# Optimization experiments

Measured on AMD Instinct MI355X. Metric: run time of the kernel, lower is better.

## Reference

```python
import jax, jax.numpy as jnp
import numpy as np

B, S, E, H, V, OOV = 128, 400, 512, 512, 50257, 50
VEXT = V + OOV


def setup_inputs() -> dict:
    key = jax.random.key(0)
    ks = jax.random.split(key, 20)
    w = lambda k, shp: (0.02 * jax.random.normal(k, shp)).astype(jnp.float32)
    return {
        'input_emb': jax.random.normal(ks[0], (B, 1, E), jnp.float32),
        'input_feed': jax.random.normal(ks[1], (B, 1, H), jnp.float32),
        'hidden': jax.random.normal(ks[2], (1, B, H), jnp.float32),
        'context': jax.random.normal(ks[3], (1, B, H), jnp.float32),
        'states': jax.random.normal(ks[4], (B, S, H), jnp.float32),
        'states_features': jax.random.normal(ks[5], (B, S, H), jnp.float32),
        'source_mask': jnp.ones((B, S), jnp.float32),
        'coverage': jnp.zeros((B, S), jnp.float32),
        'source_ids': jax.random.randint(ks[6], (B, S), 0, VEXT, jnp.int32),
        'W_ic': w(ks[7], (E, H + E)), 'b_ic': jnp.zeros((E,), jnp.float32),
        'W_ih': w(ks[8], (4 * H, E)), 'W_hh': w(ks[9], (4 * H, H)),
        'b_ih': jnp.zeros((4 * H,), jnp.float32), 'b_hh': jnp.zeros((4 * H,), jnp.float32),
        'W_dec': w(ks[10], (H, H)), 'b_att': jnp.zeros((H,), jnp.float32),
        'v_att': w(ks[11], (H,)), 'w_c': w(ks[12], (1,)),
        'W_out': w(ks[13], (H, 2 * H)), 'b_out': jnp.zeros((H,), jnp.float32),
        'W_pg': w(ks[14], (1, H)), 'b_pg': jnp.zeros((1,), jnp.float32),
        'W_v': w(ks[15], (V, H)), 'b_v': jnp.zeros((V,), jnp.float32),
    }


def reference(input_emb, input_feed, hidden, context, states, states_features,
              source_mask, coverage, source_ids,
              W_ic, b_ic, W_ih, W_hh, b_ih, b_hh,
              W_dec, b_att, v_att, w_c, W_out, b_out,
              W_pg, b_pg, W_v, b_v):
    # x = input_context(cat(input_emb, input_feed))  -> [B,1,E]
    x = jnp.concatenate([input_emb, input_feed], axis=2) @ W_ic.T + b_ic
    # single LSTM step (PyTorch gate order i,f,g,o)
    h0, c0 = hidden[0], context[0]                      # [B,H]
    gates = x[:, 0] @ W_ih.T + b_ih + h0 @ W_hh.T + b_hh
    i, f, g, o = jnp.split(gates, 4, axis=-1)
    i, f, o = jax.nn.sigmoid(i), jax.nn.sigmoid(f), jax.nn.sigmoid(o)
    c1 = f * c0 + i * jnp.tanh(g)
    h1 = o * jnp.tanh(c1)                               # rnn_output [B,H]
    # coverage attention
    dec_fea = h1 @ W_dec.T + b_att                      # [B,H]
    e = jnp.tanh(states_features + dec_fea[:, None, :] + w_c * coverage[..., None]) @ v_att  # [B,S]
    e = jnp.where(source_mask > 0, e, jnp.float32(-1e9))
    attn = jax.nn.softmax(e, axis=-1) * source_mask
    attn = attn / (attn.sum(-1, keepdims=True) + 1e-12)  # [B,S]
    ctx = jnp.einsum('bs,bsh->bh', attn, states)
    dec_out = jnp.concatenate([h1, ctx], axis=-1) @ W_out.T + b_out  # decoder_output [B,H]
    coverage_new = coverage + attn
    # pointer-generator mixing
    p_gen = jax.nn.sigmoid(dec_out @ W_pg.T + b_pg)     # [B,1]
    vocab_dist = p_gen * jax.nn.softmax(dec_out @ W_v.T + b_v, axis=-1)  # [B,V]
    ext = jnp.zeros((B, VEXT), vocab_dist.dtype).at[:, :V].set(vocab_dist)
    attn_dist = (1.0 - p_gen) * attn                    # [B,S]
    final = ext.at[jnp.arange(B)[:, None], source_ids].add(attn_dist)  # scatter_add over vocab
    final_dist = final[:, None, :]                      # [B,1,VEXT]
    return (final_dist, p_gen, attn, coverage_new, h1[None], c1[None], dec_out[:, None, :])
```

## Files before the change

### kernel.cpp

```cpp
#include <hip/hip_runtime.h>
#include <hip/hip_bf16.h>

#define B_   128
#define S_   400
#define H_   512
#define V_   50257
#define VX_  50307

#define OFF_FINAL 0
#define OFF_PGEN  6439296
#define OFF_ATTN  6439424
#define OFF_COV   6490624
#define OFF_H1    6541824
#define OFF_C1    6607360
#define OFF_DEC   6672896

typedef __attribute__((ext_vector_type(8))) short bf16x8;
typedef __attribute__((ext_vector_type(4))) float f32x4;

static __device__ __forceinline__ float sigmoid_f(float x) {
    return 1.0f / (1.0f + __expf(-x));
}
static __device__ __forceinline__ float tanh_f(float x) {
    return 1.0f - 2.0f / (__expf(2.0f * x) + 1.0f);
}
static __device__ __forceinline__ unsigned int pk2(float x, float y) {
    union { __hip_bfloat162 h; unsigned int u; } cv;
    cv.h = __float22bfloat162_rn(make_float2(x, y));
    return cv.u;
}

template <int NT>
__global__ __launch_bounds__(256) void gemm_mfma(
    const float* __restrict__ A1, const float* __restrict__ W1, int ldw1, int kwo1,
    const float* __restrict__ A2, const float* __restrict__ W2, int ldw2, int kwo2,
    const float* __restrict__ bias1, const float* __restrict__ bias2,
    float* __restrict__ C, int N)
{
    __shared__ __align__(16) unsigned short As[128 * 40];
    __shared__ __align__(16) unsigned short Ws[NT * 16 * 40];
    const int tid  = threadIdx.x;
    const int bn0  = blockIdx.x * (NT * 16);
    const int lane = tid & 63;
    const int wv   = tid >> 6;
    const int quad = lane >> 4;
    const int col  = lane & 15;

    f32x4 acc[2][NT];
#pragma unroll
    for (int i = 0; i < 2; ++i)
#pragma unroll
        for (int j = 0; j < NT; ++j) acc[i][j] = (f32x4){0.f, 0.f, 0.f, 0.f};

    const int ar = tid >> 1;
    const int ac = (tid & 1) << 4;
    const int wr = (NT == 8) ? (tid >> 1) : (tid >> 2);
    const int wc = (NT == 8) ? ((tid & 1) << 4) : ((tid & 3) << 3);
    const int wrg = (bn0 + wr < N) ? (bn0 + wr) : (N - 1);

    const int nph = (A2 != nullptr) ? 2 : 1;
    const int nsteps = nph << 4;
    const float* ApB[2];
    const float* WpB[2];
    ApB[0] = A1 + (long)ar * 512 + ac;
    WpB[0] = W1 + (long)wrg * ldw1 + kwo1 + wc;
    ApB[1] = A2 ? (A2 + (long)ar * 512 + ac) : ApB[0];
    WpB[1] = W2 ? (W2 + (long)wrg * ldw2 + kwo2 + wc) : WpB[0];

    float4 aC[4], wC[NT / 2], aN[4], wN[NT / 2];

    auto fetch = [&](int s, float4* a, float4* w) {
        const int ph = s >> 4;
        const int k0 = (s & 15) << 5;
        const float* Ap = ApB[ph] + k0;
        const float* Wp = WpB[ph] + k0;
#pragma unroll
        for (int i = 0; i < 4; ++i) a[i] = *(const float4*)(Ap + i * 4);
#pragma unroll
        for (int i = 0; i < NT / 2; ++i) w[i] = *(const float4*)(Wp + i * 4);
    };

    fetch(0, aC, wC);
    for (int s = 0; s < nsteps; ++s) {
        __syncthreads();
        uint4* apd = (uint4*)&As[ar * 40 + ac];
        apd[0] = make_uint4(pk2(aC[0].x, aC[0].y), pk2(aC[0].z, aC[0].w),
                            pk2(aC[1].x, aC[1].y), pk2(aC[1].z, aC[1].w));
        apd[1] = make_uint4(pk2(aC[2].x, aC[2].y), pk2(aC[2].z, aC[2].w),
                            pk2(aC[3].x, aC[3].y), pk2(aC[3].z, aC[3].w));
        uint4* wpd = (uint4*)&Ws[wr * 40 + wc];
        wpd[0] = make_uint4(pk2(wC[0].x, wC[0].y), pk2(wC[0].z, wC[0].w),
                            pk2(wC[1].x, wC[1].y), pk2(wC[1].z, wC[1].w));
        if (NT == 8)
            wpd[1] = make_uint4(pk2(wC[2].x, wC[2].y), pk2(wC[2].z, wC[2].w),
                                pk2(wC[3].x, wC[3].y), pk2(wC[3].z, wC[3].w));
        __syncthreads();

        if (s + 1 < nsteps) fetch(s + 1, aN, wN);

        const bf16x8 aF0 = *(const bf16x8*)&As[(wv * 32 + col) * 40 + quad * 8];
        const bf16x8 aF1 = *(const bf16x8*)&As[(wv * 32 + 16 + col) * 40 + quad * 8];
#pragma unroll
        for (int ni = 0; ni < NT; ++ni) {
            const bf16x8 bF = *(const bf16x8*)&Ws[(ni * 16 + col) * 40 + quad * 8];
            acc[0][ni] = __builtin_amdgcn_mfma_f32_16x16x32_bf16(aF0, bF, acc[0][ni], 0, 0, 0);
            acc[1][ni] = __builtin_amdgcn_mfma_f32_16x16x32_bf16(aF1, bF, acc[1][ni], 0, 0, 0);
        }
#pragma unroll
        for (int i = 0; i < 4; ++i) aC[i] = aN[i];
#pragma unroll
        for (int i = 0; i < NT / 2; ++i) wC[i] = wN[i];
    }

#pragma unroll
    for (int mi = 0; mi < 2; ++mi) {
#pragma unroll
        for (int ni = 0; ni < NT; ++ni) {
            const int n = bn0 + ni * 16 + col;
            if (n < N) {
                float bv = bias1[n];
                if (bias2) bv += bias2[n];
#pragma unroll
                for (int r = 0; r < 4; ++r) {
                    const int m = wv * 32 + mi * 16 + quad * 4 + r;
                    C[(long)m * N + n] = acc[mi][ni][r] + bv;
                }
            }
        }
    }
}

__global__ __launch_bounds__(256) void lstm_cell(
    const float* __restrict__ gates, const float* __restrict__ c0,
    float* __restrict__ h1, float* __restrict__ c1)
{
    const int idx = blockIdx.x * 256 + threadIdx.x;
    const int b = idx >> 9, h = idx & 511;
    const float* g = gates + ((long)b << 11);
    const float gi = sigmoid_f(g[h]);
    const float gf = sigmoid_f(g[h + 512]);
    const float gg = tanh_f(g[h + 1024]);
    const float go = sigmoid_f(g[h + 1536]);
    const float c = gf * c0[idx] + gi * gg;
    c1[idx] = c;
    h1[idx] = go * tanh_f(c);
}

__global__ __launch_bounds__(256) void attn_scores(
    const float* __restrict__ sfeat, const float* __restrict__ decfea,
    const float* __restrict__ cov, const float* __restrict__ wc,
    const float* __restrict__ vatt, float* __restrict__ e)
{
    const int lane = threadIdx.x & 63;
    const int pair = blockIdx.x * 4 + (threadIdx.x >> 6);
    const int b = pair / 400;
    const float cc = wc[0] * cov[pair];
    const float* sp = sfeat + ((long)pair << 9) + (lane << 3);
    const float* dp = decfea + (b << 9) + (lane << 3);
    const float* vp = vatt + (lane << 3);
    const float4 s0 = *(const float4*)sp, s1 = *(const float4*)(sp + 4);
    const float4 d0 = *(const float4*)dp, d1 = *(const float4*)(dp + 4);
    const float4 v0 = *(const float4*)vp, v1 = *(const float4*)(vp + 4);
    float acc = tanh_f(s0.x + d0.x + cc) * v0.x
              + tanh_f(s0.y + d0.y + cc) * v0.y
              + tanh_f(s0.z + d0.z + cc) * v0.z
              + tanh_f(s0.w + d0.w + cc) * v0.w
              + tanh_f(s1.x + d1.x + cc) * v1.x
              + tanh_f(s1.y + d1.y + cc) * v1.y
              + tanh_f(s1.z + d1.z + cc) * v1.z
              + tanh_f(s1.w + d1.w + cc) * v1.w;
#pragma unroll
    for (int off = 32; off > 0; off >>= 1) acc += __shfl_down(acc, off);
    if (lane == 0) e[pair] = acc;
}

__global__ __launch_bounds__(256) void attn_softmax(
    const float* __restrict__ e, const float* __restrict__ mask,
    const float* __restrict__ cov,
    float* __restrict__ attn, float* __restrict__ covnew, float* __restrict__ ctx)
{
    __shared__ float sm[4], sps[4], spms[4];
    const int b = blockIdx.x, tid = threadIdx.x;
    ctx[(b << 9) + tid] = 0.f;
    ctx[(b << 9) + 256 + tid] = 0.f;

    float vals[2], msk[2];
    float m = -3.0e38f;
#pragma unroll
    for (int it = 0; it < 2; ++it) {
        const int s = tid + (it << 8);
        float mk = 0.f, v = -3.0e38f;
        if (s < 400) {
            mk = mask[b * 400 + s];
            v = (mk > 0.f) ? e[b * 400 + s] : -1.0e9f;
        }
        vals[it] = v; msk[it] = mk;
        m = fmaxf(m, v);
    }
#pragma unroll
    for (int off = 32; off > 0; off >>= 1) m = fmaxf(m, __shfl_down(m, off));
    if ((tid & 63) == 0) sm[tid >> 6] = m;
    __syncthreads();
    const float M = fmaxf(fmaxf(sm[0], sm[1]), fmaxf(sm[2], sm[3]));

    float p[2], sp = 0.f, spm = 0.f;
#pragma unroll
    for (int it = 0; it < 2; ++it) {
        const int s = tid + (it << 8);
        float pv = 0.f;
        if (s < 400) pv = __expf(vals[it] - M);
        p[it] = pv; sp += pv; spm += pv * msk[it];
    }
#pragma unroll
    for (int off = 32; off > 0; off >>= 1) {
        sp += __shfl_down(sp, off);
        spm += __shfl_down(spm, off);
    }
    if ((tid & 63) == 0) { sps[tid >> 6] = sp; spms[tid >> 6] = spm; }
    __syncthreads();
    const float SP = sps[0] + sps[1] + sps[2] + sps[3];
    const float SPM = spms[0] + spms[1] + spms[2] + spms[3];
    const float inv = 1.0f / (SPM + 1e-12f * SP);
#pragma unroll
    for (int it = 0; it < 2; ++it) {
        const int s = tid + (it << 8);
        if (s < 400) {
            const float a = p[it] * msk[it] * inv;
            attn[b * 400 + s] = a;
            covnew[b * 400 + s] = cov[b * 400 + s] + a;
        }
    }
}

__global__ __launch_bounds__(256) void ctx_kernel(
    const float* __restrict__ attn, const float* __restrict__ states,
    float* __restrict__ ctx)
{
    const int bx = blockIdx.x;
    const int b = bx >> 2, chunk = bx & 3;
    const int tid = threadIdx.x;
    const int c = tid & 127;
    const int sh = tid >> 7;
    const int s0 = chunk * 100 + sh;
    const float* base = states + (long)b * 400 * 512;
    float4 acc = make_float4(0.f, 0.f, 0.f, 0.f);
    for (int i = 0; i < 50; ++i) {
        const int s = s0 + (i << 1);
        const float a = attn[b * 400 + s];
        const float4 st = *(const float4*)(base + (long)s * 512 + (c << 2));
        acc.x = fmaf(a, st.x, acc.x);
        acc.y = fmaf(a, st.y, acc.y);
        acc.z = fmaf(a, st.z, acc.z);
        acc.w = fmaf(a, st.w, acc.w);
    }
    float* cp = ctx + (b << 9) + (c << 2);
    atomicAdd(cp + 0, acc.x);
    atomicAdd(cp + 1, acc.y);
    atomicAdd(cp + 2, acc.z);
    atomicAdd(cp + 3, acc.w);
}

__global__ __launch_bounds__(64) void pgen_kernel(
    const float* __restrict__ dec_out, const float* __restrict__ wpg,
    const float* __restrict__ bpg, float* __restrict__ pgen)
{
    const int b = blockIdx.x, lane = threadIdx.x;
    const float* dp = dec_out + (b << 9) + (lane << 3);
    const float* wp = wpg + (lane << 3);
    const float4 d0 = *(const float4*)dp, d1 = *(const float4*)(dp + 4);
    const float4 w0 = *(const float4*)wp, w1 = *(const float4*)(wp + 4);
    float acc = d0.x * w0.x + d0.y * w0.y + d0.z * w0.z + d0.w * w0.w
              + d1.x * w1.x + d1.y * w1.y + d1.z * w1.z + d1.w * w1.w;
#pragma unroll
    for (int off = 32; off > 0; off >>= 1) acc += __shfl_down(acc, off);
    if (lane == 0) pgen[b] = sigmoid_f(acc + bpg[0]);
}

__global__ __launch_bounds__(256) void row_stats_part(
    const float* __restrict__ logits, float* __restrict__ pm, float* __restrict__ ps)
{
    __shared__ float sred[4];
    const int b = blockIdx.y, cx = blockIdx.x, tid = threadIdx.x;
    const int v0 = cx * 6283;
    const int v1 = (v0 + 6283 < V_) ? (v0 + 6283) : V_;
    const float* row = logits + (long)b * V_;

    float m = -3.0e38f;
    for (int v = v0 + tid; v < v1; v += 256) m = fmaxf(m, row[v]);
#pragma unroll
    for (int off = 32; off > 0; off >>= 1) m = fmaxf(m, __shfl_down(m, off));
    if ((tid & 63) == 0) sred[tid >> 6] = m;
    __syncthreads();
    const float M = fmaxf(fmaxf(sred[0], sred[1]), fmaxf(sred[2], sred[3]));
    __syncthreads();

    float s = 0.f;
    for (int v = v0 + tid; v < v1; v += 256) s += __expf(row[v] - M);
#pragma unroll
    for (int off = 32; off > 0; off >>= 1) s += __shfl_down(s, off);
    if ((tid & 63) == 0) sred[tid >> 6] = s;
    __syncthreads();
    if (tid == 0) {
        pm[b * 8 + cx] = M;
        ps[b * 8 + cx] = sred[0] + sred[1] + sred[2] + sred[3];
    }
}

__global__ __launch_bounds__(128) void row_stats_fin(
    const float* __restrict__ pm, const float* __restrict__ ps,
    float* __restrict__ rmax, float* __restrict__ rsum)
{
    const int b = threadIdx.x;
    float M = -3.0e38f;
#pragma unroll
    for (int i = 0; i < 8; ++i) M = fmaxf(M, pm[b * 8 + i]);
    float S = 0.f;
#pragma unroll
    for (int i = 0; i < 8; ++i) S += ps[b * 8 + i] * __expf(pm[b * 8 + i] - M);
    rmax[b] = M;
    rsum[b] = S;
}

__global__ __launch_bounds__(256) void final_write(
    const float* __restrict__ logits, const float* __restrict__ rmax,
    const float* __restrict__ rsum, const float* __restrict__ pgen,
    float* __restrict__ final)
{
    const int b = blockIdx.y;
    const int v0 = (blockIdx.x * 256 + threadIdx.x) << 2;
    if (v0 >= VX_) return;
    const float M = rmax[b];
    const float sc = pgen[b] / rsum[b];
    const float* row = logits + (long)b * V_;
    float* out = final + (long)b * VX_ + v0;
#pragma unroll
    for (int j = 0; j < 4; ++j) {
        const int v = v0 + j;
        if (v < VX_) out[j] = (v < V_) ? __expf(row[v] - M) * sc : 0.f;
    }
}

__global__ __launch_bounds__(256) void scatter_kernel(
    const int* __restrict__ ids, const float* __restrict__ attn,
    const float* __restrict__ pgen, float* __restrict__ final)
{
    const int s = blockIdx.x * 256 + threadIdx.x;
    const int b = blockIdx.y;
    if (s < 400) {
        const float v = (1.0f - pgen[b]) * attn[b * 400 + s];
        atomicAdd(final + (long)b * VX_ + ids[b * 400 + s], v);
    }
}

extern "C" void kernel_launch(void* const* d_in, const int* in_sizes, int n_in,
                              void* d_out, int out_size, void* d_ws, size_t ws_size,
                              hipStream_t stream)
{
    const float* input_emb  = (const float*)d_in[0];
    const float* input_feed = (const float*)d_in[1];
    const float* hidden     = (const float*)d_in[2];
    const float* context    = (const float*)d_in[3];
    const float* states     = (const float*)d_in[4];
    const float* sfeat      = (const float*)d_in[5];
    const float* mask       = (const float*)d_in[6];
    const float* cov        = (const float*)d_in[7];
    const int*   src_ids    = (const int*)d_in[8];
    const float* W_ic  = (const float*)d_in[9];
    const float* b_ic  = (const float*)d_in[10];
    const float* W_ih  = (const float*)d_in[11];
    const float* W_hh  = (const float*)d_in[12];
    const float* b_ih  = (const float*)d_in[13];
    const float* b_hh  = (const float*)d_in[14];
    const float* W_dec = (const float*)d_in[15];
    const float* b_att = (const float*)d_in[16];
    const float* v_att = (const float*)d_in[17];
    const float* w_c   = (const float*)d_in[18];
    const float* W_out = (const float*)d_in[19];
    const float* b_out = (const float*)d_in[20];
    const float* W_pg  = (const float*)d_in[21];
    const float* b_pg  = (const float*)d_in[22];
    const float* W_v   = (const float*)d_in[23];
    const float* b_v   = (const float*)d_in[24];

    float* out = (float*)d_out;
    float* o_final = out + OFF_FINAL;
    float* o_pgen  = out + OFF_PGEN;
    float* o_attn  = out + OFF_ATTN;
    float* o_cov   = out + OFF_COV;
    float* o_h1    = out + OFF_H1;
    float* o_c1    = out + OFF_C1;
    float* o_dec   = out + OFF_DEC;

    float* ws = (float*)d_ws;
    float* w_x      = ws;
    float* w_gates  = ws + 65536;
    float* w_decfea = ws + 327680;
    float* w_e      = ws + 393216;
    float* w_ctx    = ws + 444416;
    float* w_logits = ws + 509952;
    float* w_rmax   = ws + 6942848;
    float* w_rsum   = ws + 6942976;
    float* w_pm     = ws + 6943104;
    float* w_ps     = ws + 6944128;

    const dim3 blk(256);
    gemm_mfma<4><<<8, blk, 0, stream>>>(input_emb, W_ic, 1024, 0,
                                        input_feed, W_ic, 1024, 512,
                                        b_ic, nullptr, w_x, 512);
    gemm_mfma<4><<<32, blk, 0, stream>>>(w_x, W_ih, 512, 0,
                                         hidden, W_hh, 512, 0,
                                         b_ih, b_hh, w_gates, 2048);
    lstm_cell<<<256, blk, 0, stream>>>(w_gates, context, o_h1, o_c1);
    gemm_mfma<4><<<8, blk, 0, stream>>>(o_h1, W_dec, 512, 0,
                                        nullptr, nullptr, 0, 0,
                                        b_att, nullptr, w_decfea, 512);
    attn_scores<<<12800, blk, 0, stream>>>(sfeat, w_decfea, cov, w_c, v_att, w_e);
    attn_softmax<<<128, blk, 0, stream>>>(w_e, mask, cov, o_attn, o_cov, w_ctx);
    ctx_kernel<<<512, blk, 0, stream>>>(o_attn, states, w_ctx);
    gemm_mfma<4><<<8, blk, 0, stream>>>(o_h1, W_out, 1024, 0,
                                        w_ctx, W_out, 1024, 512,
                                        b_out, nullptr, o_dec, 512);
    pgen_kernel<<<128, dim3(64), 0, stream>>>(o_dec, W_pg, b_pg, o_pgen);
    gemm_mfma<8><<<393, blk, 0, stream>>>(o_dec, W_v, 512, 0,
                                          nullptr, nullptr, 0, 0,
                                          b_v, nullptr, w_logits, 50257);
    row_stats_part<<<dim3(8, 128), blk, 0, stream>>>(w_logits, w_pm, w_ps);
    row_stats_fin<<<1, dim3(128), 0, stream>>>(w_pm, w_ps, w_rmax, w_rsum);
    final_write<<<dim3(50, 128), blk, 0, stream>>>(w_logits, w_rmax, w_rsum, o_pgen, o_final);
    scatter_kernel<<<dim3(2, 128), blk, 0, stream>>>(src_ids, o_attn, o_pgen, o_final);
}
```

Measured before the change: 521.8 us.

## Split-K small GEMMs, fuse gates with LSTM cell, fold p_gen into decoder GEMM

Adds split-K over gridDim.y for the small 128-row GEMMs (input_context, W_dec, W_out), accumulating with atomics into buffers zeroed by a new kernel. The gates GEMM and LSTM cell are fused so each block computes the i/f/g/o columns for 32 hidden units and applies the cell directly, removing the gates round trip. p_gen's dot product is folded into the W_out GEMM epilogue via atomics, the row_stats_fin kernel is merged into final_write, and the vocab GEMM switches from NT=8 to NT=4 with twice the blocks. The aim is more parallelism for tiny GEMMs and fewer launches, at the cost of float atomics (nondeterministic summation order) and an extra zeroing launch.

Result: faster. 492.1 us (-5.7%).

```diff
diff --git a/kernel.cpp b/kernel.cpp
--- a/kernel.cpp
+++ b/kernel.cpp
@@ -30,12 +30,22 @@
     return cv.u;
 }
 
+__global__ __launch_bounds__(256) void zero_bufs(
+    float* __restrict__ a, float* __restrict__ b, float* __restrict__ c,
+    float* __restrict__ d)
+{
+    const int i = blockIdx.x * 256 + threadIdx.x;
+    a[i] = 0.f; b[i] = 0.f; c[i] = 0.f;
+    if (i < 128) d[i] = 0.f;
+}
+
 template <int NT>
 __global__ __launch_bounds__(256) void gemm_mfma(
     const float* __restrict__ A1, const float* __restrict__ W1, int ldw1, int kwo1,
     const float* __restrict__ A2, const float* __restrict__ W2, int ldw2, int kwo2,
-    const float* __restrict__ bias1, const float* __restrict__ bias2,
-    float* __restrict__ C, int N)
+    const float* __restrict__ bias1,
+    float* __restrict__ C, int N,
+    const float* __restrict__ wpg, float* __restrict__ pgen_acc)
 {
     __shared__ __align__(16) unsigned short As[128 * 40];
     __shared__ __align__(16) unsigned short Ws[NT * 16 * 40];
@@ -58,8 +68,11 @@
     const int wc = (NT == 8) ? ((tid & 1) << 4) : ((tid & 3) << 3);
     const int wrg = (bn0 + wr < N) ? (bn0 + wr) : (N - 1);
 
-    const int nph = (A2 != nullptr) ? 2 : 1;
-    const int nsteps = nph << 4;
+    const int Ktot = (A2 != nullptr) ? 1024 : 512;
+    const int KC   = Ktot / gridDim.y;
+    const int kg0  = blockIdx.y * KC;
+    const int nsteps = KC >> 5;
+
     const float* ApB[2];
     const float* WpB[2];
     ApB[0] = A1 + (long)ar * 512 + ac;
@@ -70,8 +83,9 @@
     float4 aC[4], wC[NT / 2], aN[4], wN[NT / 2];
 
     auto fetch = [&](int s, float4* a, float4* w) {
-        const int ph = s >> 4;
-        const int k0 = (s & 15) << 5;
+        const int kg = kg0 + (s << 5);
+        const int ph = kg >> 9;
+        const int k0 = kg & 511;
         const float* Ap = ApB[ph] + k0;
         const float* Wp = WpB[ph] + k0;
 #pragma unroll
@@ -112,38 +126,143 @@
         for (int i = 0; i < NT / 2; ++i) wC[i] = wN[i];
     }
 
+    const bool split = (gridDim.y > 1);
+    const bool addb  = (!split) || (blockIdx.y == 0);
+    float pgp[2][4];
+#pragma unroll
+    for (int i = 0; i < 2; ++i)
+#pragma unroll
+        for (int r = 0; r < 4; ++r) pgp[i][r] = 0.f;
+
 #pragma unroll
     for (int mi = 0; mi < 2; ++mi) {
 #pragma unroll
         for (int ni = 0; ni < NT; ++ni) {
             const int n = bn0 + ni * 16 + col;
             if (n < N) {
-                float bv = bias1[n];
-                if (bias2) bv += bias2[n];
+                const float bv = addb ? bias1[n] : 0.f;
+                const float wpv = wpg ? wpg[n] : 0.f;
 #pragma unroll
                 for (int r = 0; r < 4; ++r) {
                     const int m = wv * 32 + mi * 16 + quad * 4 + r;
-                    C[(long)m * N + n] = acc[mi][ni][r] + bv;
+                    const float v = acc[mi][ni][r] + bv;
+                    if (split) atomicAdd(&C[(long)m * N + n], v);
+                    else       C[(long)m * N + n] = v;
+                    pgp[mi][r] += v * wpv;
                 }
             }
         }
     }
-}
-
-__global__ __launch_bounds__(256) void lstm_cell(
-    const float* __restrict__ gates, const float* __restrict__ c0,
+    if (wpg) {
+#pragma unroll
+        for (int mi = 0; mi < 2; ++mi)
+#pragma unroll
+            for (int r = 0; r < 4; ++r) {
+                float v = pgp[mi][r];
+                v += __shfl_xor(v, 1); v += __shfl_xor(v, 2);
+                v += __shfl_xor(v, 4); v += __shfl_xor(v, 8);
+                if (col == 0) {
+                    const int m = wv * 32 + mi * 16 + quad * 4 + r;
+                    atomicAdd(&pgen_acc[m], v);
+                }
+            }
+    }
+}
+
+__global__ __launch_bounds__(256) void gates_lstm(
+    const float* __restrict__ x, const float* __restrict__ h0,
+    const float* __restrict__ Wih, const float* __restrict__ Whh,
+    const float* __restrict__ bih, const float* __restrict__ bhh,
+    const float* __restrict__ c0,
     float* __restrict__ h1, float* __restrict__ c1)
 {
-    const int idx = blockIdx.x * 256 + threadIdx.x;
-    const int b = idx >> 9, h = idx & 511;
-    const float* g = gates + ((long)b << 11);
-    const float gi = sigmoid_f(g[h]);
-    const float gf = sigmoid_f(g[h + 512]);
-    const float gg = tanh_f(g[h + 1024]);
-    const float go = sigmoid_f(g[h + 1536]);
-    const float c = gf * c0[idx] + gi * gg;
-    c1[idx] = c;
-    h1[idx] = go * tanh_f(c);
+    __shared__ __align__(16) unsigned short As[128 * 40];
+    __shared__ __align__(16) unsigned short Ws[128 * 40];
+    const int tid  = threadIdx.x;
+    const int bh0  = blockIdx.x * 32;
+    const int lane = tid & 63;
+    const int wv   = tid >> 6;
+    const int quad = lane >> 4;
+    const int col  = lane & 15;
+
+    f32x4 acc[2][8];
+#pragma unroll
+    for (int i = 0; i < 2; ++i)
+#pragma unroll
+        for (int j = 0; j < 8; ++j) acc[i][j] = (f32x4){0.f, 0.f, 0.f, 0.f};
+
+    const int ar = tid >> 1;
+    const int ac = (tid & 1) << 4;
+    const int wr = tid >> 1;
+    const int wc = (tid & 1) << 4;
+    const int wrow = ((wr >> 5) << 9) + bh0 + (wr & 31);
+
+    const float* ApB[2] = { x + (long)ar * 512 + ac, h0 + (long)ar * 512 + ac };
+    const float* WpB[2] = { Wih + (long)wrow * 512 + wc, Whh + (long)wrow * 512 + wc };
+
+    float4 aC[4], wC[4], aN[4], wN[4];
+    auto fetch = [&](int s, float4* a, float4* w) {
+        const int ph = s >> 4;
+        const int k0 = (s & 15) << 5;
+        const float* Ap = ApB[ph] + k0;
+        const float* Wp = WpB[ph] + k0;
+#pragma unroll
+        for (int i = 0; i < 4; ++i) a[i] = *(const float4*)(Ap + i * 4);
+#pragma unroll
+        for (int i = 0; i < 4; ++i) w[i] = *(const float4*)(Wp + i * 4);
+    };
+
+    fetch(0, aC, wC);
+    for (int s = 0; s < 32; ++s) {
+        __syncthreads();
+        uint4* apd = (uint4*)&As[ar * 40 + ac];
+        apd[0] = make_uint4(pk2(aC[0].x, aC[0].y), pk2(aC[0].z, aC[0].w),
+                            pk2(aC[1].x, aC[1].y), pk2(aC[1].z, aC[1].w));
+        apd[1] = make_uint4(pk2(aC[2].x, aC[2].y), pk2(aC[2].z, aC[2].w),
+                            pk2(aC[3].x, aC[3].y), pk2(aC[3].z, aC[3].w));
+        uint4* wpd = (uint4*)&Ws[wr * 40 + wc];
+        wpd[0] = make_uint4(pk2(wC[0].x, wC[0].y), pk2(wC[0].z, wC[0].w),
+                            pk2(wC[1].x, wC[1].y), pk2(wC[1].z, wC[1].w));
+        wpd[1] = make_uint4(pk2(wC[2].x, wC[2].y), pk2(wC[2].z, wC[2].w),
+                            pk2(wC[3].x, wC[3].y), pk2(wC[3].z, wC[3].w));
+        __syncthreads();
+
+        if (s + 1 < 32) fetch(s + 1, aN, wN);
+
+        const bf16x8 aF0 = *(const bf16x8*)&As[(wv * 32 + col) * 40 + quad * 8];
+        const bf16x8 aF1 = *(const bf16x8*)&As[(wv * 32 + 16 + col) * 40 + quad * 8];
+#pragma unroll
+        for (int ni = 0; ni < 8; ++ni) {
+            const bf16x8 bF = *(const bf16x8*)&Ws[(ni * 16 + col) * 40 + quad * 8];
+            acc[0][ni] = __builtin_amdgcn_mfma_f32_16x16x32_bf16(aF0, bF, acc[0][ni], 0, 0, 0);
+            acc[1][ni] = __builtin_amdgcn_mfma_f32_16x16x32_bf16(aF1, bF, acc[1][ni], 0, 0, 0);
+        }
+#pragma unroll
+        for (int i = 0; i < 4; ++i) { aC[i] = aN[i]; wC[i] = wN[i]; }
+    }
+
+#pragma unroll
+    for (int mi = 0; mi < 2; ++mi) {
+#pragma unroll
+        for (int par = 0; par < 2; ++par) {
+            const int h = bh0 + par * 16 + col;
+            const float bi = bih[h]        + bhh[h];
+            const float bf = bih[512 + h]  + bhh[512 + h];
+            const float bg = bih[1024 + h] + bhh[1024 + h];
+            const float bo = bih[1536 + h] + bhh[1536 + h];
+#pragma unroll
+            for (int r = 0; r < 4; ++r) {
+                const int m = wv * 32 + mi * 16 + quad * 4 + r;
+                const float iv = sigmoid_f(acc[mi][par + 0][r] + bi);
+                const float fv = sigmoid_f(acc[mi][par + 2][r] + bf);
+                const float gv = tanh_f(acc[mi][par + 4][r] + bg);
+                const float ov = sigmoid_f(acc[mi][par + 6][r] + bo);
+                const float c = fv * c0[m * 512 + h] + iv * gv;
+                c1[m * 512 + h] = c;
+                h1[m * 512 + h] = ov * tanh_f(c);
+            }
+        }
+    }
 }
 
 __global__ __launch_bounds__(256) void attn_scores(
@@ -260,22 +379,6 @@
     atomicAdd(cp + 3, acc.w);
 }
 
-__global__ __launch_bounds__(64) void pgen_kernel(
-    const float* __restrict__ dec_out, const float* __restrict__ wpg,
-    const float* __restrict__ bpg, float* __restrict__ pgen)
-{
-    const int b = blockIdx.x, lane = threadIdx.x;
-    const float* dp = dec_out + (b << 9) + (lane << 3);
-    const float* wp = wpg + (lane << 3);
-    const float4 d0 = *(const float4*)dp, d1 = *(const float4*)(dp + 4);
-    const float4 w0 = *(const float4*)wp, w1 = *(const float4*)(wp + 4);
-    float acc = d0.x * w0.x + d0.y * w0.y + d0.z * w0.z + d0.w * w0.w
-              + d1.x * w1.x + d1.y * w1.y + d1.z * w1.z + d1.w * w1.w;
-#pragma unroll
-    for (int off = 32; off > 0; off >>= 1) acc += __shfl_down(acc, off);
-    if (lane == 0) pgen[b] = sigmoid_f(acc + bpg[0]);
-}
-
 __global__ __launch_bounds__(256) void row_stats_part(
     const float* __restrict__ logits, float* __restrict__ pm, float* __restrict__ ps)
 {
@@ -306,31 +409,25 @@
     }
 }
 
-__global__ __launch_bounds__(128) void row_stats_fin(
-    const float* __restrict__ pm, const float* __restrict__ ps,
-    float* __restrict__ rmax, float* __restrict__ rsum)
-{
-    const int b = threadIdx.x;
+__global__ __launch_bounds__(256) void final_write(
+    const float* __restrict__ logits, const float* __restrict__ pm,
+    const float* __restrict__ ps, const float* __restrict__ pgen_acc,
+    const float* __restrict__ bpg, float* __restrict__ final,
+    float* __restrict__ o_pgen)
+{
+    const int b = blockIdx.y;
     float M = -3.0e38f;
 #pragma unroll
     for (int i = 0; i < 8; ++i) M = fmaxf(M, pm[b * 8 + i]);
     float S = 0.f;
 #pragma unroll
     for (int i = 0; i < 8; ++i) S += ps[b * 8 + i] * __expf(pm[b * 8 + i] - M);
-    rmax[b] = M;
-    rsum[b] = S;
-}
-
-__global__ __launch_bounds__(256) void final_write(
-    const float* __restrict__ logits, const float* __restrict__ rmax,
-    const float* __restrict__ rsum, const float* __restrict__ pgen,
-    float* __restrict__ final)
-{
-    const int b = blockIdx.y;
+    const float pg = sigmoid_f(pgen_acc[b] + bpg[0]);
+    if (blockIdx.x == 0 && threadIdx.x == 0) o_pgen[b] = pg;
+
     const int v0 = (blockIdx.x * 256 + threadIdx.x) << 2;
     if (v0 >= VX_) return;
-    const float M = rmax[b];
-    const float sc = pgen[b] / rsum[b];
+    const float sc = pg / S;
     const float* row = logits + (long)b * V_;
     float* out = final + (long)b * VX_ + v0;
 #pragma unroll
@@ -393,39 +490,35 @@
 
     float* ws = (float*)d_ws;
     float* w_x      = ws;
-    float* w_gates  = ws + 65536;
     float* w_decfea = ws + 327680;
     float* w_e      = ws + 393216;
     float* w_ctx    = ws + 444416;
     float* w_logits = ws + 509952;
-    float* w_rmax   = ws + 6942848;
-    float* w_rsum   = ws + 6942976;
     float* w_pm     = ws + 6943104;
     float* w_ps     = ws + 6944128;
+    float* w_pga    = ws + 6945152;
 
     const dim3 blk(256);
-    gemm_mfma<4><<<8, blk, 0, stream>>>(input_emb, W_ic, 1024, 0,
-                                        input_feed, W_ic, 1024, 512,
-                                        b_ic, nullptr, w_x, 512);
-    gemm_mfma<4><<<32, blk, 0, stream>>>(w_x, W_ih, 512, 0,
-                                         hidden, W_hh, 512, 0,
-                                         b_ih, b_hh, w_gates, 2048);
-    lstm_cell<<<256, blk, 0, stream>>>(w_gates, context, o_h1, o_c1);
-    gemm_mfma<4><<<8, blk, 0, stream>>>(o_h1, W_dec, 512, 0,
-                                        nullptr, nullptr, 0, 0,
-                                        b_att, nullptr, w_decfea, 512);
+    zero_bufs<<<256, blk, 0, stream>>>(w_x, w_decfea, o_dec, w_pga);
+    gemm_mfma<4><<<dim3(8, 8), blk, 0, stream>>>(
+        input_emb, W_ic, 1024, 0, input_feed, W_ic, 1024, 512,
+        b_ic, w_x, 512, nullptr, nullptr);
+    gates_lstm<<<16, blk, 0, stream>>>(w_x, hidden, W_ih, W_hh, b_ih, b_hh,
+                                       context, o_h1, o_c1);
+    gemm_mfma<4><<<dim3(8, 4), blk, 0, stream>>>(
+        o_h1, W_dec, 512, 0, nullptr, nullptr, 0, 0,
+        b_att, w_decfea, 512, nullptr, nullptr);
     attn_scores<<<12800, blk, 0, stream>>>(sfeat, w_decfea, cov, w_c, v_att, w_e);
     attn_softmax<<<128, blk, 0, stream>>>(w_e, mask, cov, o_attn, o_cov, w_ctx);
     ctx_kernel<<<512, blk, 0, stream>>>(o_attn, states, w_ctx);
-    gemm_mfma<4><<<8, blk, 0, stream>>>(o_h1, W_out, 1024, 0,
-                                        w_ctx, W_out, 1024, 512,
-                                        b_out, nullptr, o_dec, 512);
-    pgen_kernel<<<128, dim3(64), 0, stream>>>(o_dec, W_pg, b_pg, o_pgen);
-    gemm_mfma<8><<<393, blk, 0, stream>>>(o_dec, W_v, 512, 0,
-                                          nullptr, nullptr, 0, 0,
-                                          b_v, nullptr, w_logits, 50257);
+    gemm_mfma<4><<<dim3(8, 8), blk, 0, stream>>>(
+        o_h1, W_out, 1024, 0, w_ctx, W_out, 1024, 512,
+        b_out, o_dec, 512, W_pg, w_pga);
+    gemm_mfma<4><<<dim3(786, 1), blk, 0, stream>>>(
+        o_dec, W_v, 512, 0, nullptr, nullptr, 0, 0,
+        b_v, w_logits, 50257, nullptr, nullptr);
     row_stats_part<<<dim3(8, 128), blk, 0, stream>>>(w_logits, w_pm, w_ps);
-    row_stats_fin<<<1, dim3(128), 0, stream>>>(w_pm, w_ps, w_rmax, w_rsum);
-    final_write<<<dim3(50, 128), blk, 0, stream>>>(w_logits, w_rmax, w_rsum, o_pgen, o_final);
+    final_write<<<dim3(50, 128), blk, 0, stream>>>(w_logits, w_pm, w_ps, w_pga,
+                                                   b_pg, o_final, o_pgen);
     scatter_kernel<<<dim3(2, 128), blk, 0, stream>>>(src_ids, o_attn, o_pgen, o_final);
 }
```
